# Performance work log

Measured on AMD Instinct MI355X. Metric: run time of the kernel, lower is better.

Reference implementation:

```python
import jax, jax.numpy as jnp
import numpy as np
from jax import lax

T = 262144
D = 128          # feature dim of X[t]
H = 256          # cell hidden dim


def setup_inputs() -> dict:
    key = jax.random.key(0)
    k_x, k_w1, k_w2 = jax.random.split(key, 3)
    X = jax.random.normal(k_x, (T, D), dtype=jnp.float32)
    # MLP cell params: z_next = tanh(W2 @ tanh(W1 @ [x; z] + b1) + b2)
    W1 = jax.random.normal(k_w1, (H, D + 1), dtype=jnp.float32) / np.sqrt(D + 1)
    b1 = jnp.zeros((H,), dtype=jnp.float32)
    W2 = jax.random.normal(k_w2, (1, H), dtype=jnp.float32) / np.sqrt(H)
    b2 = jnp.zeros((1,), dtype=jnp.float32)
    return {"X": X, "W1": W1, "b1": b1, "W2": W2, "b2": b2}


def reference(X, W1, b1, W2, b2):
    # Faithful to RecurrentRunner.forward: Z[0] = 0, Z[t+1] = cell(X[t], Z[t])
    # for t in 0..T-2; X[T-1] is never consumed.
    def step(z, x):
        inp = jnp.concatenate([x, z[None]])          # [D+1]
        h = jnp.tanh(W1 @ inp + b1)                  # [H]
        z_next = jnp.tanh(W2 @ h + b2)[0]            # scalar
        return z_next, z_next

    z0 = jnp.zeros((), dtype=X.dtype)
    _, zs = lax.scan(step, z0, X[:-1])               # [T-1]
    return jnp.concatenate([jnp.zeros((1,), dtype=X.dtype), zs])  # [T]
```

## Files before the change

### kernel.cpp

```cpp
#include <hip/hip_runtime.h>
#include <hip/hip_fp16.h>

#define T_TOTAL 262144
#define DD 128
#define HH 256

#define P1_BLOCKS 2048
#define TILE_T 16
#define TPB 8
#define TBLK (TPB * TILE_T)
#define NW 8

#define P2_CHUNKS 2048
#define P2_L (T_TOTAL / P2_CHUNKS)
#define BURN 40

typedef _Float16 half8 __attribute__((ext_vector_type(8)));
typedef float f32x4 __attribute__((ext_vector_type(4)));

__device__ __forceinline__ float fast_tanh(float x) {
    float e = __expf(2.0f * x);
#if __has_builtin(__builtin_amdgcn_rcpf)
    float r = __builtin_amdgcn_rcpf(e + 1.0f);
#else
    float r = 1.0f / (e + 1.0f);
#endif
    return 1.0f - 2.0f * r;
}

__device__ __forceinline__ float swz16(float v) {
    return __int_as_float(__builtin_amdgcn_ds_swizzle(__float_as_int(v), 0x401F));
}
__device__ __forceinline__ float bperm(int xaddr, float v) {
    return __int_as_float(__builtin_amdgcn_ds_bpermute(xaddr, __float_as_int(v)));
}

__device__ __forceinline__ half8 cvt8(float4 a, float4 b) {
    half8 h;
    h[0] = (_Float16)a.x; h[1] = (_Float16)a.y;
    h[2] = (_Float16)a.z; h[3] = (_Float16)a.w;
    h[4] = (_Float16)b.x; h[5] = (_Float16)b.y;
    h[6] = (_Float16)b.z; h[7] = (_Float16)b.w;
    return h;
}

__device__ __forceinline__ half8 pack8(float4 a, float4 b) {
    const unsigned u0 = __builtin_bit_cast(unsigned, __builtin_amdgcn_cvt_pkrtz(a.x, a.y));
    const unsigned u1 = __builtin_bit_cast(unsigned, __builtin_amdgcn_cvt_pkrtz(a.z, a.w));
    const unsigned u2 = __builtin_bit_cast(unsigned, __builtin_amdgcn_cvt_pkrtz(b.x, b.y));
    const unsigned u3 = __builtin_bit_cast(unsigned, __builtin_amdgcn_cvt_pkrtz(b.z, b.w));
    unsigned int uv[4] = {u0, u1, u2, u3};
    return __builtin_bit_cast(half8, *(uint4*)uv);
}

__global__ __launch_bounds__(512)
void coeff_kernel(const float* __restrict__ X, const float* __restrict__ W1,
                  const float* __restrict__ b1, const float* __restrict__ W2,
                  const float* __restrict__ b2, float2* __restrict__ cs)
{
    const int tid = threadIdx.x;
    const int wid = tid >> 6;
    const int l   = tid & 63;
    const int r16 = l & 15;
    const int g   = l >> 4;
    const int jb  = wid * 32;

    __shared__ __align__(16) _Float16 xh[TBLK][DD];
    __shared__ float2 slab[NW][TBLK];

    const int t0 = blockIdx.x * TBLK;

    {
        #pragma unroll
        for (int m = 0; m < 4; ++m) {
            const int G   = m * 512 + tid;
            const int row = G >> 4;
            const int gc  = (G & 15) ^ (row & 7);
            const float* src = X + (long long)(t0 + row) * DD + (G & 15) * 8;
            const float4 a = *(const float4*)(src);
            const float4 b = *(const float4*)(src + 4);
            *(half8*)&xh[row][gc * 8] = pack8(a, b);
        }
    }

    half8 wf[2][4];
    f32x4 b1v[2], q0v[2], q1v[2];
    #pragma unroll
    for (int js = 0; js < 2; ++js) {
        {
            const int j = jb + js * 16 + r16;
            const float* wr = W1 + j * (DD + 1);
            #pragma unroll
            for (int ks = 0; ks < 4; ++ks) {
                const float4 a = *(const float4*)(wr + g * 8 + ks * 32);
                const float4 b = *(const float4*)(wr + g * 8 + ks * 32 + 4);
                wf[js][ks] = cvt8(a, b);
            }
        }
        const int j0 = jb + js * 16 + g * 4;
        b1v[js] = *(const f32x4*)(b1 + j0);
        const f32x4 w2v = *(const f32x4*)(W2 + j0);
        f32x4 wzv;
        #pragma unroll
        for (int r = 0; r < 4; ++r) wzv[r] = W1[(j0 + r) * (DD + 1) + DD];
        q0v[js] = w2v;
        q1v[js] = w2v * wzv;
    }
    const float b2s = b2[0];
    const int xaddr = ((l ^ 32) << 2);

    __syncthreads();

    for (int tile = 0; tile < TPB; ++tile) {
        f32x4 acc[2] = {b1v[0], b1v[1]};
        #pragma unroll
        for (int ks = 0; ks < 4; ++ks) {
            const int gc = (g + 4 * ks) ^ (r16 & 7);
            const half8 xf = *(const half8*)&xh[tile * TILE_T + r16][gc * 8];
            acc[0] = __builtin_amdgcn_mfma_f32_16x16x32_f16(wf[0][ks], xf, acc[0], 0, 0, 0);
            acc[1] = __builtin_amdgcn_mfma_f32_16x16x32_f16(wf[1][ks], xf, acc[1], 0, 0, 0);
        }

        float c0 = 0.f, c1 = 0.f;
        #pragma unroll
        for (int js = 0; js < 2; ++js) {
            #pragma unroll
            for (int r = 0; r < 4; ++r) {
                const float f = fast_tanh(acc[js][r]);
                const float d = 1.0f - f * f;
                c0 = fmaf(q0v[js][r], f, c0);
                c1 = fmaf(q1v[js][r], d, c1);
            }
        }
        c0 += swz16(c0); c1 += swz16(c1);
        c0 += bperm(xaddr, c0); c1 += bperm(xaddr, c1);
        if (l < 16)
            slab[wid][tile * TILE_T + l] = make_float2(c0, c1);
    }

    __syncthreads();
    if (tid < TBLK) {
        float2 s = slab[0][tid];
        #pragma unroll
        for (int w = 1; w < NW; ++w) {
            const float2 a = slab[w][tid];
            s.x += a.x; s.y += a.y;
        }
        s.x += b2s;
        cs[t0 + tid] = s;
    }
}

__global__ __launch_bounds__(64)
void chain_kernel(const float2* __restrict__ cs, float* __restrict__ out)
{
    const int c   = blockIdx.x;
    const int tid = threadIdx.x;
    const int s0     = (c == 0) ? 0 : c * P2_L - BURN;
    const int t_end  = min((c + 1) * P2_L, T_TOTAL - 1);
    const int n      = t_end - s0;
    const int wstart = c * P2_L;
    const int skip   = wstart - s0;

    __shared__ float2 cl[P2_L + BURN];
    __shared__ float  zb[P2_L + BURN];
    for (int i = tid; i < n; i += 64) cl[i] = cs[s0 + i];
    __syncthreads();

    float z = 0.0f;
    #pragma unroll 4
    for (int i = 0; i < n; ++i) {
        const float2 k = cl[i];
        const float u = fmaf(k.y, z, k.x);
        z = fast_tanh(u);
        if (tid == 0) zb[i] = z;
    }
    __syncthreads();

    if (c == 0 && tid == 0) out[0] = 0.0f;
    for (int i = tid; i + skip < n; i += 64)
        out[wstart + 1 + i] = zb[skip + i];
}

extern "C" void kernel_launch(void* const* d_in, const int* in_sizes, int n_in,
                              void* d_out, int out_size, void* d_ws, size_t ws_size,
                              hipStream_t stream) {
    const float* X  = (const float*)d_in[0];
    const float* W1 = (const float*)d_in[1];
    const float* b1 = (const float*)d_in[2];
    const float* W2 = (const float*)d_in[3];
    const float* b2 = (const float*)d_in[4];
    float* out = (float*)d_out;
    float2* cs = (float2*)d_ws;
    (void)in_sizes; (void)n_in; (void)out_size; (void)ws_size;

    coeff_kernel<<<P1_BLOCKS, 512, 0, stream>>>(X, W1, b1, W2, b2, cs);
    chain_kernel<<<P2_CHUNKS, 64, 0, stream>>>(cs, out);
}
```

Measured before the change: 66.85 us.

## Prepack W1 to fp16 once and loop coeff blocks over four tiles

Adds a small pre-kernel that converts W1 into a packed fp16 fragment layout, plus a separate array for its last column. coeff_kernel now runs 512 blocks, each looping over 4 super-tiles of 128 timesteps and loading the weight fragments into registers once. This spreads the per-block weight load and conversion over more timesteps. In exchange it adds a kernel launch, serialises the X load with compute inside each block without double buffering, and leaves fewer blocks for latency hiding.

After: 65.55 us. Within noise of the previous version (-1.9%).

```diff
diff --git a/kernel.cpp b/kernel.cpp
--- a/kernel.cpp
+++ b/kernel.cpp
@@ -5,7 +5,8 @@
 #define DD 128
 #define HH 256
 
-#define P1_BLOCKS 2048
+#define P1_BLOCKS 512
+#define SUPT 4
 #define TILE_T 16
 #define TPB 8
 #define TBLK (TPB * TILE_T)
@@ -14,6 +15,10 @@
 #define P2_CHUNKS 2048
 #define P2_L (T_TOTAL / P2_CHUNKS)
 #define BURN 40
+
+#define CS_BYTES   (T_TOTAL * 8)
+#define WPACK_OFF  CS_BYTES
+#define WZ_OFF     (WPACK_OFF + HH * DD * 2)
 
 typedef _Float16 half8 __attribute__((ext_vector_type(8)));
 typedef float f32x4 __attribute__((ext_vector_type(4)));
@@ -53,10 +58,25 @@
     return __builtin_bit_cast(half8, *(uint4*)uv);
 }
 
+__global__ __launch_bounds__(128)
+void pack_kernel(const float* __restrict__ W1, half8* __restrict__ wpack,
+                 float* __restrict__ wz)
+{
+    const int gid = blockIdx.x * 128 + threadIdx.x;
+    const int row = gid >> 4;
+    const int seg = gid & 15;
+    const float* src = W1 + row * (DD + 1) + seg * 8;
+    const float4 a = *(const float4*)(src);
+    const float4 b = *(const float4*)(src + 4);
+    wpack[gid] = cvt8(a, b);
+    if (seg == 0) wz[row] = W1[row * (DD + 1) + DD];
+}
+
 __global__ __launch_bounds__(512)
-void coeff_kernel(const float* __restrict__ X, const float* __restrict__ W1,
-                  const float* __restrict__ b1, const float* __restrict__ W2,
-                  const float* __restrict__ b2, float2* __restrict__ cs)
+void coeff_kernel(const float* __restrict__ X, const float* __restrict__ b1,
+                  const float* __restrict__ W2, const float* __restrict__ b2,
+                  const half8* __restrict__ wpack, const float* __restrict__ wz,
+                  float2* __restrict__ cs)
 {
     const int tid = threadIdx.x;
     const int wid = tid >> 6;
@@ -68,9 +88,28 @@
     __shared__ __align__(16) _Float16 xh[TBLK][DD];
     __shared__ float2 slab[NW][TBLK];
 
-    const int t0 = blockIdx.x * TBLK;
-
-    {
+    half8 wf[2][4];
+    f32x4 b1v[2], q0v[2], q1v[2];
+    #pragma unroll
+    for (int js = 0; js < 2; ++js) {
+        const int j = jb + js * 16 + r16;
+        #pragma unroll
+        for (int ks = 0; ks < 4; ++ks)
+            wf[js][ks] = wpack[j * 16 + (g + 4 * ks)];
+        const int j0 = jb + js * 16 + g * 4;
+        b1v[js] = *(const f32x4*)(b1 + j0);
+        const f32x4 w2v = *(const f32x4*)(W2 + j0);
+        const f32x4 wzv = *(const f32x4*)(wz + j0);
+        q0v[js] = w2v;
+        q1v[js] = w2v * wzv;
+    }
+    const float b2s = b2[0];
+    const int xaddr = ((l ^ 32) << 2);
+
+    for (int st = 0; st < SUPT; ++st) {
+        const int t0 = (blockIdx.x * SUPT + st) * TBLK;
+
+        __syncthreads();
         #pragma unroll
         for (int m = 0; m < 4; ++m) {
             const int G   = m * 512 + tid;
@@ -81,73 +120,46 @@
             const float4 b = *(const float4*)(src + 4);
             *(half8*)&xh[row][gc * 8] = pack8(a, b);
         }
-    }
-
-    half8 wf[2][4];
-    f32x4 b1v[2], q0v[2], q1v[2];
-    #pragma unroll
-    for (int js = 0; js < 2; ++js) {
-        {
-            const int j = jb + js * 16 + r16;
-            const float* wr = W1 + j * (DD + 1);
+        __syncthreads();
+
+        for (int tile = 0; tile < TPB; ++tile) {
+            f32x4 acc[2] = {b1v[0], b1v[1]};
             #pragma unroll
             for (int ks = 0; ks < 4; ++ks) {
-                const float4 a = *(const float4*)(wr + g * 8 + ks * 32);
-                const float4 b = *(const float4*)(wr + g * 8 + ks * 32 + 4);
-                wf[js][ks] = cvt8(a, b);
+                const int gc = (g + 4 * ks) ^ (r16 & 7);
+                const half8 xf = *(const half8*)&xh[tile * TILE_T + r16][gc * 8];
+                acc[0] = __builtin_amdgcn_mfma_f32_16x16x32_f16(wf[0][ks], xf, acc[0], 0, 0, 0);
+                acc[1] = __builtin_amdgcn_mfma_f32_16x16x32_f16(wf[1][ks], xf, acc[1], 0, 0, 0);
             }
+
+            float c0 = 0.f, c1 = 0.f;
+            #pragma unroll
+            for (int js = 0; js < 2; ++js) {
+                #pragma unroll
+                for (int r = 0; r < 4; ++r) {
+                    const float f = fast_tanh(acc[js][r]);
+                    const float d = 1.0f - f * f;
+                    c0 = fmaf(q0v[js][r], f, c0);
+                    c1 = fmaf(q1v[js][r], d, c1);
+                }
+            }
+            c0 += swz16(c0); c1 += swz16(c1);
+            c0 += bperm(xaddr, c0); c1 += bperm(xaddr, c1);
+            if (l < 16)
+                slab[wid][tile * TILE_T + l] = make_float2(c0, c1);
         }
-        const int j0 = jb + js * 16 + g * 4;
-        b1v[js] = *(const f32x4*)(b1 + j0);
-        const f32x4 w2v = *(const f32x4*)(W2 + j0);
-        f32x4 wzv;
-        #pragma unroll
-        for (int r = 0; r < 4; ++r) wzv[r] = W1[(j0 + r) * (DD + 1) + DD];
-        q0v[js] = w2v;
-        q1v[js] = w2v * wzv;
-    }
-    const float b2s = b2[0];
-    const int xaddr = ((l ^ 32) << 2);
-
-    __syncthreads();
-
-    for (int tile = 0; tile < TPB; ++tile) {
-        f32x4 acc[2] = {b1v[0], b1v[1]};
-        #pragma unroll
-        for (int ks = 0; ks < 4; ++ks) {
-            const int gc = (g + 4 * ks) ^ (r16 & 7);
-            const half8 xf = *(const half8*)&xh[tile * TILE_T + r16][gc * 8];
-            acc[0] = __builtin_amdgcn_mfma_f32_16x16x32_f16(wf[0][ks], xf, acc[0], 0, 0, 0);
-            acc[1] = __builtin_amdgcn_mfma_f32_16x16x32_f16(wf[1][ks], xf, acc[1], 0, 0, 0);
+
+        __syncthreads();
+        if (tid < TBLK) {
+            float2 s = slab[0][tid];
+            #pragma unroll
+            for (int w = 1; w < NW; ++w) {
+                const float2 a = slab[w][tid];
+                s.x += a.x; s.y += a.y;
+            }
+            s.x += b2s;
+            cs[t0 + tid] = s;
         }
-
-        float c0 = 0.f, c1 = 0.f;
-        #pragma unroll
-        for (int js = 0; js < 2; ++js) {
-            #pragma unroll
-            for (int r = 0; r < 4; ++r) {
-                const float f = fast_tanh(acc[js][r]);
-                const float d = 1.0f - f * f;
-                c0 = fmaf(q0v[js][r], f, c0);
-                c1 = fmaf(q1v[js][r], d, c1);
-            }
-        }
-        c0 += swz16(c0); c1 += swz16(c1);
-        c0 += bperm(xaddr, c0); c1 += bperm(xaddr, c1);
-        if (l < 16)
-            slab[wid][tile * TILE_T + l] = make_float2(c0, c1);
-    }
-
-    __syncthreads();
-    if (tid < TBLK) {
-        float2 s = slab[0][tid];
-        #pragma unroll
-        for (int w = 1; w < NW; ++w) {
-            const float2 a = slab[w][tid];
-            s.x += a.x; s.y += a.y;
-        }
-        s.x += b2s;
-        cs[t0 + tid] = s;
     }
 }
 
@@ -191,9 +203,13 @@
     const float* W2 = (const float*)d_in[3];
     const float* b2 = (const float*)d_in[4];
     float* out = (float*)d_out;
-    float2* cs = (float2*)d_ws;
+    char* ws = (char*)d_ws;
+    float2* cs   = (float2*)ws;
+    half8* wpack = (half8*)(ws + WPACK_OFF);
+    float* wzv   = (float*)(ws + WZ_OFF);
     (void)in_sizes; (void)n_in; (void)out_size; (void)ws_size;
 
-    coeff_kernel<<<P1_BLOCKS, 512, 0, stream>>>(X, W1, b1, W2, b2, cs);
+    pack_kernel<<<32, 128, 0, stream>>>(W1, wpack, wzv);
+    coeff_kernel<<<P1_BLOCKS, 512, 0, stream>>>(X, b1, W2, b2, wpack, wzv, cs);
     chain_kernel<<<P2_CHUNKS, 64, 0, stream>>>(cs, out);
 }
```
